# Kernel optimization log

Hardware: AMD Instinct MI355X
Metric: run time of the kernel (lower is better)

## Reference

```python
import jax, jax.numpy as jnp
import numpy as np

B, L_DEC, L_ENC = 4, 1024, 1024
D_MODEL, D_INNER, N_HEAD, D_K, D_V = 512, 256, 8, 64, 64
TEMP = D_K ** 0.5
EPS = 1e-6


def _layernorm(x, g, b):
    mu = jnp.mean(x, axis=-1, keepdims=True)
    var = jnp.mean(jnp.square(x - mu), axis=-1, keepdims=True)
    return (x - mu) * jax.lax.rsqrt(var + EPS) * g + b


def _mha(x_q, x_kv, Wq, Wk, Wv, Wfc, ln_g, ln_b, mask):
    # Faithful to source: only the query input is layer-normed; k/v use raw x_kv.
    resid = x_q
    qn = _layernorm(x_q, ln_g, ln_b)
    # Stacked per-head projections: Wq/Wk/Wv are [H, d_k, d_model]
    q = jnp.einsum('bld,hkd->bhlk', qn, Wq) / TEMP   # [B,H,Lq,dk]
    k = jnp.einsum('bld,hkd->bhlk', x_kv, Wk)        # [B,H,Lk,dk]
    v = jnp.einsum('bld,hkd->bhlk', x_kv, Wv)        # [B,H,Lk,dv]
    scores = jnp.einsum('bhqd,bhkd->bhqk', q, k)     # [B,H,Lq,Lk]
    if mask is not None:
        scores = jnp.where(mask[:, None, :, :] == 0, -jnp.inf, scores)
    attn = jax.nn.softmax(scores, axis=-1)
    out = jnp.einsum('bhqk,bhkd->bhqd', attn, v)     # [B,H,Lq,dv]
    Bq, H, Lq, dv = out.shape
    out = out.transpose(0, 2, 1, 3).reshape(Bq, Lq, H * dv)
    return out @ Wfc.T + resid


def _ffn(x, W1, b1, W2, b2, ln_g, ln_b):
    resid = x
    h = _layernorm(x, ln_g, ln_b)
    h = jax.nn.relu(h @ W1.T + b1) @ W2.T + b2
    return h + resid


def setup_inputs() -> dict:
    key = jax.random.key(0)
    ks = jax.random.split(key, 20)
    s = 0.02
    dec_input = jax.random.normal(ks[0], (B, L_DEC, D_MODEL), jnp.float32)
    enc_output = jax.random.normal(ks[1], (B, L_ENC, D_MODEL), jnp.float32)
    slf_attn_mask = jnp.tril(jnp.ones((1, L_DEC, L_DEC), jnp.int32))  # causal
    p = {}
    for i, pre in enumerate(['slf', 'enc']):
        base = 2 + i * 4
        p[f'{pre}_Wq'] = jax.random.normal(ks[base], (N_HEAD, D_K, D_MODEL), jnp.float32) * s
        p[f'{pre}_Wk'] = jax.random.normal(ks[base + 1], (N_HEAD, D_K, D_MODEL), jnp.float32) * s
        p[f'{pre}_Wv'] = jax.random.normal(ks[base + 2], (N_HEAD, D_V, D_MODEL), jnp.float32) * s
        p[f'{pre}_Wfc'] = jax.random.normal(ks[base + 3], (D_MODEL, N_HEAD * D_V), jnp.float32) * s
        p[f'{pre}_ln_g'] = jnp.ones((D_MODEL,), jnp.float32)
        p[f'{pre}_ln_b'] = jnp.zeros((D_MODEL,), jnp.float32)
    p['ffn_W1'] = jax.random.normal(ks[10], (D_INNER, D_MODEL), jnp.float32) * s
    p['ffn_b1'] = jnp.zeros((D_INNER,), jnp.float32)
    p['ffn_W2'] = jax.random.normal(ks[11], (D_MODEL, D_INNER), jnp.float32) * s
    p['ffn_b2'] = jnp.zeros((D_MODEL,), jnp.float32)
    p['ffn_ln_g'] = jnp.ones((D_MODEL,), jnp.float32)
    p['ffn_ln_b'] = jnp.zeros((D_MODEL,), jnp.float32)
    return {'dec_input': dec_input, 'enc_output': enc_output,
            'slf_attn_mask': slf_attn_mask, **p}


def reference(dec_input, enc_output,
              slf_Wq, slf_Wk, slf_Wv, slf_Wfc, slf_ln_g, slf_ln_b,
              enc_Wq, enc_Wk, enc_Wv, enc_Wfc, enc_ln_g, enc_ln_b,
              ffn_W1, ffn_b1, ffn_W2, ffn_b2, ffn_ln_g, ffn_ln_b,
              slf_attn_mask):
    x = _mha(dec_input, dec_input, slf_Wq, slf_Wk, slf_Wv, slf_Wfc,
             slf_ln_g, slf_ln_b, slf_attn_mask)
    x = _mha(x, enc_output, enc_Wq, enc_Wk, enc_Wv, enc_Wfc,
             enc_ln_g, enc_ln_b, None)
    x = _ffn(x, ffn_W1, ffn_b1, ffn_W2, ffn_b2, ffn_ln_g, ffn_ln_b)
    return x
```

## Files before the change

kernel.cpp:

```cpp
#include <hip/hip_runtime.h>
#include <hip/hip_bf16.h>
#include <math.h>

#define DMODEL 512
#define NHEAD  8
#define DHEAD  64

typedef __attribute__((ext_vector_type(8))) short bf16x8;
typedef __attribute__((ext_vector_type(4))) float f32x4;
typedef __attribute__((ext_vector_type(4))) short short4v;

static __device__ inline short f2bf(float f) {
    __hip_bfloat16 h = __float2bfloat16(f);
    return *reinterpret_cast<short*>(&h);
}

#define GLOAD_LDS16(gp, lp)                                                      \
    __builtin_amdgcn_global_load_lds(                                            \
        (const __attribute__((address_space(1))) unsigned int*)(gp),             \
        (__attribute__((address_space(3))) unsigned int*)(lp), 16, 0, 0)

struct CvtArgs {
    const float* src[10];
    short*       dst[10];
    int          n[10];
};

__global__ __launch_bounds__(256) void cvt_kernel(CvtArgs args) {
    int t = blockIdx.y;
    int idx = (blockIdx.x * 256 + threadIdx.x) * 8;
    if (idx >= args.n[t]) return;
    const float* s = args.src[t] + idx;
    float4 a = *(const float4*)s;
    float4 b = *(const float4*)(s + 4);
    bf16x8 o;
    o[0] = f2bf(a.x); o[1] = f2bf(a.y); o[2] = f2bf(a.z); o[3] = f2bf(a.w);
    o[4] = f2bf(b.x); o[5] = f2bf(b.y); o[6] = f2bf(b.z); o[7] = f2bf(b.w);
    *(bf16x8*)(args.dst[t] + idx) = o;
}

__global__ __launch_bounds__(256) void ln_kernel(const float* __restrict__ X,
                                                 const float* __restrict__ gam,
                                                 const float* __restrict__ bet,
                                                 short* __restrict__ Y,
                                                 const float* __restrict__ C1s,
                                                 short* __restrict__ C1d,
                                                 const float* __restrict__ C2s,
                                                 short* __restrict__ C2d) {
    int row = blockIdx.x * 4 + (threadIdx.x >> 6);
    int tid = threadIdx.x & 63;
    const float* x = X + (size_t)row * DMODEL;
    float4 a = *(const float4*)(x + tid * 4);
    float4 b = *(const float4*)(x + 256 + tid * 4);
    float sum = a.x + a.y + a.z + a.w + b.x + b.y + b.z + b.w;
    float sq  = a.x*a.x + a.y*a.y + a.z*a.z + a.w*a.w
              + b.x*b.x + b.y*b.y + b.z*b.z + b.w*b.w;
#pragma unroll
    for (int off = 1; off < 64; off <<= 1) {
        sum += __shfl_xor(sum, off);
        sq  += __shfl_xor(sq, off);
    }
    float mu  = sum * (1.0f / DMODEL);
    float var = sq * (1.0f / DMODEL) - mu * mu;
    float r   = rsqrtf(var + 1e-6f);

    float4 g1 = *(const float4*)(gam + tid * 4);
    float4 c1 = *(const float4*)(bet + tid * 4);
    float4 g2 = *(const float4*)(gam + 256 + tid * 4);
    float4 c2 = *(const float4*)(bet + 256 + tid * 4);
    short4v y1, y2;
    y1.x = f2bf((a.x - mu) * r * g1.x + c1.x);
    y1.y = f2bf((a.y - mu) * r * g1.y + c1.y);
    y1.z = f2bf((a.z - mu) * r * g1.z + c1.z);
    y1.w = f2bf((a.w - mu) * r * g1.w + c1.w);
    y2.x = f2bf((b.x - mu) * r * g2.x + c2.x);
    y2.y = f2bf((b.y - mu) * r * g2.y + c2.y);
    y2.z = f2bf((b.z - mu) * r * g2.z + c2.z);
    y2.w = f2bf((b.w - mu) * r * g2.w + c2.w);
    short* y = Y + (size_t)row * DMODEL;
    *(short4v*)(y + tid * 4)       = y1;
    *(short4v*)(y + 256 + tid * 4) = y2;

    if (C1s) {
        short4v d1, d2;
        d1.x = f2bf(a.x); d1.y = f2bf(a.y); d1.z = f2bf(a.z); d1.w = f2bf(a.w);
        d2.x = f2bf(b.x); d2.y = f2bf(b.y); d2.z = f2bf(b.z); d2.w = f2bf(b.w);
        short* d = C1d + (size_t)row * DMODEL;
        *(short4v*)(d + tid * 4)       = d1;
        *(short4v*)(d + 256 + tid * 4) = d2;
    }
    if (C2s) {
        const float* e = C2s + (size_t)row * DMODEL;
        float4 ea = *(const float4*)(e + tid * 4);
        float4 eb = *(const float4*)(e + 256 + tid * 4);
        short4v d1, d2;
        d1.x = f2bf(ea.x); d1.y = f2bf(ea.y); d1.z = f2bf(ea.z); d1.w = f2bf(ea.w);
        d2.x = f2bf(eb.x); d2.y = f2bf(eb.y); d2.z = f2bf(eb.z); d2.w = f2bf(eb.w);
        short* d = C2d + (size_t)row * DMODEL;
        *(short4v*)(d + tid * 4)       = d1;
        *(short4v*)(d + 256 + tid * 4) = d2;
    }
}

struct GJobs {
    const short* A[3];
    const short* W[3];
    const float* bias[3];
    const float* resid[3];
    void*        C[3];
    int M[3], N[3], K[3];
    float scale[3];
    int relu[3], obf[3], nblk[3];
};

__global__ __launch_bounds__(256) void gemm_bf16(GJobs jb) {
    __shared__ short As[2][64 * 64];
    __shared__ short Bs[2][64 * 64];

    int bid = blockIdx.x, j = 0;
    while (j < 2 && bid >= jb.nblk[j]) { bid -= jb.nblk[j]; ++j; }
    const short* __restrict__ A = jb.A[j];
    const short* __restrict__ W = jb.W[j];
    const int N = jb.N[j], K = jb.K[j];
    const int nbx = N >> 6;
    const int tn = (bid % nbx) * 64;
    const int tm = (bid / nbx) * 64;

    const int tid  = threadIdx.x;
    const int w    = tid >> 6;
    const int l    = tid & 63;
    const int lq   = l & 15;
    const int g    = l >> 4;
    const int wm   = (w >> 1) * 32;
    const int wn   = (w & 1) * 32;
    const int lrow = l >> 3;
    const int lsl  = l & 7;

    f32x4 acc[2][2];
#pragma unroll
    for (int i = 0; i < 2; ++i)
#pragma unroll
        for (int jj = 0; jj < 2; ++jj)
            acc[i][jj] = (f32x4){0.f, 0.f, 0.f, 0.f};

#define GSTAGE(buf, koff)                                                        \
    do {                                                                         \
        _Pragma("unroll")                                                        \
        for (int i_ = 0; i_ < 2; ++i_) {                                         \
            int row_ = i_ * 32 + w * 8 + lrow;                                   \
            int slot_ = lsl ^ (row_ & 7);                                        \
            GLOAD_LDS16(A + (size_t)(tm + row_) * K + (koff) + slot_ * 8,        \
                        As[buf] + i_ * 2048 + w * 512);                          \
            GLOAD_LDS16(W + (size_t)(tn + row_) * K + (koff) + slot_ * 8,        \
                        Bs[buf] + i_ * 2048 + w * 512);                          \
        }                                                                        \
    } while (0)

    GSTAGE(0, 0);
    int buf = 0;
#pragma unroll 1
    for (int k0 = 0; k0 < K; k0 += 64, buf ^= 1) {
        __syncthreads();
        if (k0 + 64 < K) GSTAGE(buf ^ 1, k0 + 64);
#pragma unroll
        for (int ks = 0; ks < 2; ++ks) {
            const int sl = ((ks * 4 + g) ^ (lq & 7)) * 8;
            bf16x8 af[2], bfv[2];
#pragma unroll
            for (int i = 0; i < 2; ++i) {
                af[i]  = *(const bf16x8*)&As[buf][(wm + i * 16 + lq) * 64 + sl];
                bfv[i] = *(const bf16x8*)&Bs[buf][(wn + i * 16 + lq) * 64 + sl];
            }
#pragma unroll
            for (int i = 0; i < 2; ++i)
#pragma unroll
                for (int jj = 0; jj < 2; ++jj)
                    acc[i][jj] = __builtin_amdgcn_mfma_f32_16x16x32_bf16(
                        af[i], bfv[jj], acc[i][jj], 0, 0, 0);
        }
    }
#undef GSTAGE

    const float* bias  = jb.bias[j];
    const float* resid = jb.resid[j];
    const float scale  = jb.scale[j];
    const int relu = jb.relu[j], obf = jb.obf[j];
#pragma unroll
    for (int i = 0; i < 2; ++i) {
#pragma unroll
        for (int r = 0; r < 4; ++r) {
            int row = tm + wm + i * 16 + g * 4 + r;
#pragma unroll
            for (int jj = 0; jj < 2; ++jj) {
                int col = tn + wn + jj * 16 + lq;
                float v = acc[i][jj][r] * scale;
                if (bias)  v += bias[col];
                if (resid) v += resid[(size_t)row * N + col];
                if (relu)  v = fmaxf(v, 0.f);
                if (obf) ((short*)jb.C[j])[(size_t)row * N + col] = f2bf(v);
                else     ((float*)jb.C[j])[(size_t)row * N + col] = v;
            }
        }
    }
}

__global__ __launch_bounds__(256) void attn_mfma_kernel(
        const short* __restrict__ Q, const short* __restrict__ K,
        const short* __restrict__ V, short* __restrict__ O,
        int Lq, int Lk, int causal, int qs, int kvs) {
    __shared__ short Kt[64 * 64];
    __shared__ short Vt[64][72];
    __shared__ short Pb[4][16][72];

    const int tid  = threadIdx.x;
    const int wave = tid >> 6;
    const int lane = tid & 63;
    const int lq   = lane & 15;
    const int g    = lane >> 4;
    const int bh   = blockIdx.y;
    const int b = bh >> 3, h = bh & 7;
    const int band = causal ? ((bh < 16) ? (int)blockIdx.x : (15 - (int)blockIdx.x))
                            : (int)blockIdx.x;
    const int qt = band * 4 + wave;
    const int q0 = qt * 16;
    const float NEG = -__builtin_inff();

    size_t qoff = (size_t)(b * Lq + q0 + lq) * qs + h * DHEAD;
    bf16x8 qf0 = *(const bf16x8*)(Q + qoff + g * 8);
    bf16x8 qf1 = *(const bf16x8*)(Q + qoff + 32 + g * 8);

    f32x4 o[4] = {{0,0,0,0},{0,0,0,0},{0,0,0,0},{0,0,0,0}};
    f32x4 lacc = {0.f, 0.f, 0.f, 0.f};

    bf16x8 ones;
    {
        short ov = (lq == 0) ? (short)0x3F80 : (short)0;
#pragma unroll
        for (int i = 0; i < 8; ++i) ones[i] = ov;
    }

    const int nkt = causal ? (band + 1) : (Lk >> 6);
    const int lrow = lane >> 3;
    const int lsl  = lane & 7;
    const int va = tid & 31;
    const int vd = (tid >> 5) * 8;

#pragma unroll 1
    for (int kt = 0; kt < nkt; ++kt) {
        __syncthreads();
#pragma unroll
        for (int i = 0; i < 2; ++i) {
            int row = i * 32 + wave * 8 + lrow;
            int slot = lsl ^ (row & 7);
            GLOAD_LDS16(K + (size_t)(b * Lk + kt * 64 + row) * kvs + h * DHEAD + slot * 8,
                        Kt + i * 2048 + wave * 512);
        }
        {
            size_t gb = (size_t)(b * Lk + kt * 64 + 2 * va) * kvs + h * DHEAD + vd;
            bf16x8 v0 = *(const bf16x8*)(V + gb);
            bf16x8 v1 = *(const bf16x8*)(V + gb + kvs);
#pragma unroll
            for (int i = 0; i < 8; ++i) {
                unsigned p = (unsigned short)v0[i] | ((unsigned)(unsigned short)v1[i] << 16);
                *(unsigned*)&Vt[vd + i][2 * va] = p;
            }
        }
        __syncthreads();

        f32x4 s[4];
#pragma unroll
        for (int sub = 0; sub < 4; ++sub) {
            int rr = sub * 16 + lq;
            const int sl0 = ((0 + g) ^ (lq & 7)) * 8;
            const int sl1 = ((4 + g) ^ (lq & 7)) * 8;
            bf16x8 kf0 = *(const bf16x8*)&Kt[rr * 64 + sl0];
            bf16x8 kf1 = *(const bf16x8*)&Kt[rr * 64 + sl1];
            f32x4 a = {0.f, 0.f, 0.f, 0.f};
            a = __builtin_amdgcn_mfma_f32_16x16x32_bf16(kf0, qf0, a, 0, 0, 0);
            a = __builtin_amdgcn_mfma_f32_16x16x32_bf16(kf1, qf1, a, 0, 0, 0);
            s[sub] = a;
        }
        if (causal && kt == nkt - 1) {
            int qg = q0 + lq;
#pragma unroll
            for (int sub = 0; sub < 4; ++sub) {
#pragma unroll
                for (int r = 0; r < 4; ++r) {
                    int kg = kt * 64 + sub * 16 + g * 4 + r;
                    if (kg > qg) s[sub][r] = NEG;
                }
            }
        }

#pragma unroll
        for (int sub = 0; sub < 4; ++sub) {
            short4v p4;
            p4.x = f2bf(__expf(fminf(s[sub][0], 60.f)));
            p4.y = f2bf(__expf(fminf(s[sub][1], 60.f)));
            p4.z = f2bf(__expf(fminf(s[sub][2], 60.f)));
            p4.w = f2bf(__expf(fminf(s[sub][3], 60.f)));
            *(short4v*)&Pb[wave][lq][sub * 16 + g * 4] = p4;
        }
        bf16x8 pf0 = *(const bf16x8*)&Pb[wave][lq][g * 8];
        bf16x8 pf1 = *(const bf16x8*)&Pb[wave][lq][32 + g * 8];

#pragma unroll
        for (int dc = 0; dc < 4; ++dc) {
            bf16x8 vf0 = *(const bf16x8*)&Vt[dc * 16 + lq][g * 8];
            bf16x8 vf1 = *(const bf16x8*)&Vt[dc * 16 + lq][32 + g * 8];
            o[dc] = __builtin_amdgcn_mfma_f32_16x16x32_bf16(pf0, vf0, o[dc], 0, 0, 0);
            o[dc] = __builtin_amdgcn_mfma_f32_16x16x32_bf16(pf1, vf1, o[dc], 0, 0, 0);
        }
        lacc = __builtin_amdgcn_mfma_f32_16x16x32_bf16(pf0, ones, lacc, 0, 0, 0);
        lacc = __builtin_amdgcn_mfma_f32_16x16x32_bf16(pf1, ones, lacc, 0, 0, 0);
    }

#pragma unroll
    for (int r = 0; r < 4; ++r) {
        float lr = __shfl(lacc[r], g << 4);
        float inv = 1.f / lr;
        size_t ob = (size_t)(b * Lq + q0 + g * 4 + r) * qs + h * DHEAD + lq;
        O[ob + 0]  = f2bf(o[0][r] * inv);
        O[ob + 16] = f2bf(o[1][r] * inv);
        O[ob + 32] = f2bf(o[2][r] * inv);
        O[ob + 48] = f2bf(o[3][r] * inv);
    }
}

static void launch_gemm(GJobs& jb, int njobs, hipStream_t stream) {
    int total = 0;
    for (int i = 0; i < 3; ++i) { if (i >= njobs) jb.nblk[i] = 0; total += jb.nblk[i]; }
    gemm_bf16<<<total, 256, 0, stream>>>(jb);
}

extern "C" void kernel_launch(void* const* d_in, const int* in_sizes, int n_in,
                              void* d_out, int out_size, void* d_ws, size_t ws_size,
                              hipStream_t stream) {
    const float* dec       = (const float*)d_in[0];
    const float* enc       = (const float*)d_in[1];
    const float* slf_Wq    = (const float*)d_in[3];
    const float* slf_Wk    = (const float*)d_in[4];
    const float* slf_Wv    = (const float*)d_in[5];
    const float* slf_Wfc   = (const float*)d_in[6];
    const float* slf_ln_g  = (const float*)d_in[7];
    const float* slf_ln_b  = (const float*)d_in[8];
    const float* enc_Wq    = (const float*)d_in[9];
    const float* enc_Wk    = (const float*)d_in[10];
    const float* enc_Wv    = (const float*)d_in[11];
    const float* enc_Wfc   = (const float*)d_in[12];
    const float* enc_ln_g  = (const float*)d_in[13];
    const float* enc_ln_b  = (const float*)d_in[14];
    const float* ffn_W1    = (const float*)d_in[15];
    const float* ffn_b1    = (const float*)d_in[16];
    const float* ffn_W2    = (const float*)d_in[17];
    const float* ffn_b2    = (const float*)d_in[18];
    const float* ffn_ln_g  = (const float*)d_in[19];
    const float* ffn_ln_b  = (const float*)d_in[20];
    float* out = (float*)d_out;

    const int Bb = 4, L = 1024, M = Bb * L;
    const size_t NE = (size_t)M * DMODEL;
    const int WQN = NHEAD * DHEAD * DMODEL;
    float* ws = (float*)d_ws;
    float* x1 = ws;
    float* x2 = ws + NE;
    short* kv16e = (short*)x2;
    short* sb = (short*)(ws + 2 * NE);
    short* dec16 = sb;               sb += NE;
    short* enc16 = sb;               sb += NE;
    short* qn16  = sb;               sb += NE;
    short* q16   = sb;               sb += NE;
    short* ao16  = sb;               sb += NE;
    short* kv16  = sb;               sb += 2 * NE;
    short* h16   = sb;               sb += NE / 2;
    short* wq_s  = sb;               sb += WQN;
    short* wkv_s = sb;               sb += 2 * WQN;
    short* wfc_s = sb;               sb += WQN;
    short* wq_e  = sb;               sb += WQN;
    short* wkv_e = sb;               sb += 2 * WQN;
    short* wfc_e = sb;               sb += WQN;
    short* w1_16 = sb;               sb += 256 * DMODEL;
    short* w2_16 = sb;               sb += DMODEL * 256;

    CvtArgs ca;
    ca.src[0] = slf_Wq;  ca.dst[0] = wq_s;          ca.n[0] = WQN;
    ca.src[1] = slf_Wk;  ca.dst[1] = wkv_s;         ca.n[1] = WQN;
    ca.src[2] = slf_Wv;  ca.dst[2] = wkv_s + WQN;   ca.n[2] = WQN;
    ca.src[3] = slf_Wfc; ca.dst[3] = wfc_s;         ca.n[3] = WQN;
    ca.src[4] = enc_Wq;  ca.dst[4] = wq_e;          ca.n[4] = WQN;
    ca.src[5] = enc_Wk;  ca.dst[5] = wkv_e;         ca.n[5] = WQN;
    ca.src[6] = enc_Wv;  ca.dst[6] = wkv_e + WQN;   ca.n[6] = WQN;
    ca.src[7] = enc_Wfc; ca.dst[7] = wfc_e;         ca.n[7] = WQN;
    ca.src[8] = ffn_W1;  ca.dst[8] = w1_16;         ca.n[8] = 256 * DMODEL;
    ca.src[9] = ffn_W2;  ca.dst[9] = w2_16;         ca.n[9] = DMODEL * 256;
    cvt_kernel<<<dim3(128, 10), 256, 0, stream>>>(ca);

    dim3 attn_grid(L / 64, Bb * NHEAD);
    const int NB512  = (M / 64) * (512 / 64);
    const int NB1024 = (M / 64) * (1024 / 64);
    const int NB256  = (M / 64) * (256 / 64);

    ln_kernel<<<M / 4, 256, 0, stream>>>(dec, slf_ln_g, slf_ln_b, qn16,
                                         dec, dec16, enc, enc16);
    {
        GJobs jb = {};
        jb.A[0] = qn16;  jb.W[0] = wq_s;  jb.C[0] = q16;
        jb.M[0] = M; jb.N[0] = 512;  jb.K[0] = 512; jb.scale[0] = 0.125f;
        jb.obf[0] = 1; jb.nblk[0] = NB512;
        jb.A[1] = dec16; jb.W[1] = wkv_s; jb.C[1] = kv16;
        jb.M[1] = M; jb.N[1] = 1024; jb.K[1] = 512; jb.scale[1] = 1.f;
        jb.obf[1] = 1; jb.nblk[1] = NB1024;
        jb.A[2] = enc16; jb.W[2] = wkv_e; jb.C[2] = kv16e;
        jb.M[2] = M; jb.N[2] = 1024; jb.K[2] = 512; jb.scale[2] = 1.f;
        jb.obf[2] = 1; jb.nblk[2] = NB1024;
        launch_gemm(jb, 3, stream);
    }
    attn_mfma_kernel<<<attn_grid, 256, 0, stream>>>(q16, kv16, kv16 + 512, ao16,
                                                    L, L, 1, DMODEL, 1024);
    {
        GJobs jb = {};
        jb.A[0] = ao16; jb.W[0] = wfc_s; jb.resid[0] = dec; jb.C[0] = x1;
        jb.M[0] = M; jb.N[0] = 512; jb.K[0] = 512; jb.scale[0] = 1.f;
        jb.obf[0] = 0; jb.nblk[0] = NB512;
        launch_gemm(jb, 1, stream);
    }

    ln_kernel<<<M / 4, 256, 0, stream>>>(x1, enc_ln_g, enc_ln_b, qn16,
                                         nullptr, nullptr, nullptr, nullptr);
    {
        GJobs jb = {};
        jb.A[0] = qn16; jb.W[0] = wq_e; jb.C[0] = q16;
        jb.M[0] = M; jb.N[0] = 512; jb.K[0] = 512; jb.scale[0] = 0.125f;
        jb.obf[0] = 1; jb.nblk[0] = NB512;
        launch_gemm(jb, 1, stream);
    }
    attn_mfma_kernel<<<attn_grid, 256, 0, stream>>>(q16, kv16e, kv16e + 512, ao16,
                                                    L, L, 0, DMODEL, 1024);
    {
        GJobs jb = {};
        jb.A[0] = ao16; jb.W[0] = wfc_e; jb.resid[0] = x1; jb.C[0] = x2;
        jb.M[0] = M; jb.N[0] = 512; jb.K[0] = 512; jb.scale[0] = 1.f;
        jb.obf[0] = 0; jb.nblk[0] = NB512;
        launch_gemm(jb, 1, stream);
    }

    ln_kernel<<<M / 4, 256, 0, stream>>>(x2, ffn_ln_g, ffn_ln_b, qn16,
                                         nullptr, nullptr, nullptr, nullptr);
    {
        GJobs jb = {};
        jb.A[0] = qn16; jb.W[0] = w1_16; jb.bias[0] = ffn_b1; jb.C[0] = h16;
        jb.M[0] = M; jb.N[0] = 256; jb.K[0] = 512; jb.scale[0] = 1.f;
        jb.relu[0] = 1; jb.obf[0] = 1; jb.nblk[0] = NB256;
        launch_gemm(jb, 1, stream);
    }
    {
        GJobs jb = {};
        jb.A[0] = h16; jb.W[0] = w2_16; jb.bias[0] = ffn_b2; jb.resid[0] = x2;
        jb.C[0] = out;
        jb.M[0] = M; jb.N[0] = 512; jb.K[0] = 256; jb.scale[0] = 1.f;
        jb.obf[0] = 0; jb.nblk[0] = NB512;
        launch_gemm(jb, 1, stream);
    }
}
```

Measured before the change: 255.6 us.

## Enlarge GEMM tiles, double-buffer attention K/V, use exp2 with folded log2e

GEMM tiles grow from 64x64 to 128x128, with each wave now computing a 64x64 sub-tile of 4x4 MFMAs. The aim is more operand reuse per LDS load, at the cost of more registers and many fewer blocks (e.g. 128 for N=512 with M=4096), which may underfill the device. The attention kernel double-buffers K and V in shared memory, prefetching the next tile while computing the current one, which drops one barrier per iteration. The softmax uses exp2 with log2(e) folded into the Q projection scale.

```diff
diff --git a/kernel.cpp b/kernel.cpp
--- a/kernel.cpp
+++ b/kernel.cpp
@@ -114,39 +114,39 @@
 };
 
 __global__ __launch_bounds__(256) void gemm_bf16(GJobs jb) {
-    __shared__ short As[2][64 * 64];
-    __shared__ short Bs[2][64 * 64];
+    __shared__ short As[2][128 * 64];
+    __shared__ short Bs[2][128 * 64];
 
     int bid = blockIdx.x, j = 0;
     while (j < 2 && bid >= jb.nblk[j]) { bid -= jb.nblk[j]; ++j; }
     const short* __restrict__ A = jb.A[j];
     const short* __restrict__ W = jb.W[j];
     const int N = jb.N[j], K = jb.K[j];
-    const int nbx = N >> 6;
-    const int tn = (bid % nbx) * 64;
-    const int tm = (bid / nbx) * 64;
+    const int nbx = N >> 7;
+    const int tn = (bid % nbx) * 128;
+    const int tm = (bid / nbx) * 128;
 
     const int tid  = threadIdx.x;
     const int w    = tid >> 6;
     const int l    = tid & 63;
     const int lq   = l & 15;
     const int g    = l >> 4;
-    const int wm   = (w >> 1) * 32;
-    const int wn   = (w & 1) * 32;
+    const int w0   = (w >> 1) * 64;
+    const int w1   = (w & 1) * 64;
     const int lrow = l >> 3;
     const int lsl  = l & 7;
 
-    f32x4 acc[2][2];
-#pragma unroll
-    for (int i = 0; i < 2; ++i)
-#pragma unroll
-        for (int jj = 0; jj < 2; ++jj)
+    f32x4 acc[4][4];
+#pragma unroll
+    for (int i = 0; i < 4; ++i)
+#pragma unroll
+        for (int jj = 0; jj < 4; ++jj)
             acc[i][jj] = (f32x4){0.f, 0.f, 0.f, 0.f};
 
 #define GSTAGE(buf, koff)                                                        \
     do {                                                                         \
         _Pragma("unroll")                                                        \
-        for (int i_ = 0; i_ < 2; ++i_) {                                         \
+        for (int i_ = 0; i_ < 4; ++i_) {                                         \
             int row_ = i_ * 32 + w * 8 + lrow;                                   \
             int slot_ = lsl ^ (row_ & 7);                                        \
             GLOAD_LDS16(A + (size_t)(tm + row_) * K + (koff) + slot_ * 8,        \
@@ -165,16 +165,16 @@
 #pragma unroll
         for (int ks = 0; ks < 2; ++ks) {
             const int sl = ((ks * 4 + g) ^ (lq & 7)) * 8;
-            bf16x8 af[2], bfv[2];
-#pragma unroll
-            for (int i = 0; i < 2; ++i) {
-                af[i]  = *(const bf16x8*)&As[buf][(wm + i * 16 + lq) * 64 + sl];
-                bfv[i] = *(const bf16x8*)&Bs[buf][(wn + i * 16 + lq) * 64 + sl];
+            bf16x8 af[4], bfv[4];
+#pragma unroll
+            for (int i = 0; i < 4; ++i) {
+                af[i]  = *(const bf16x8*)&As[buf][(w0 + i * 16 + lq) * 64 + sl];
+                bfv[i] = *(const bf16x8*)&Bs[buf][(w1 + i * 16 + lq) * 64 + sl];
             }
 #pragma unroll
-            for (int i = 0; i < 2; ++i)
-#pragma unroll
-                for (int jj = 0; jj < 2; ++jj)
+            for (int i = 0; i < 4; ++i)
+#pragma unroll
+                for (int jj = 0; jj < 4; ++jj)
                     acc[i][jj] = __builtin_amdgcn_mfma_f32_16x16x32_bf16(
                         af[i], bfv[jj], acc[i][jj], 0, 0, 0);
         }
@@ -186,13 +186,13 @@
     const float scale  = jb.scale[j];
     const int relu = jb.relu[j], obf = jb.obf[j];
 #pragma unroll
-    for (int i = 0; i < 2; ++i) {
+    for (int i = 0; i < 4; ++i) {
 #pragma unroll
         for (int r = 0; r < 4; ++r) {
-            int row = tm + wm + i * 16 + g * 4 + r;
-#pragma unroll
-            for (int jj = 0; jj < 2; ++jj) {
-                int col = tn + wn + jj * 16 + lq;
+            int row = tm + w0 + i * 16 + g * 4 + r;
+#pragma unroll
+            for (int jj = 0; jj < 4; ++jj) {
+                int col = tn + w1 + jj * 16 + lq;
                 float v = acc[i][jj][r] * scale;
                 if (bias)  v += bias[col];
                 if (resid) v += resid[(size_t)row * N + col];
@@ -208,8 +208,8 @@
         const short* __restrict__ Q, const short* __restrict__ K,
         const short* __restrict__ V, short* __restrict__ O,
         int Lq, int Lk, int causal, int qs, int kvs) {
-    __shared__ short Kt[64 * 64];
-    __shared__ short Vt[64][72];
+    __shared__ short Kt[2][64 * 64];
+    __shared__ short Vt[2][64][72];
     __shared__ short Pb[4][16][72];
 
     const int tid  = threadIdx.x;
@@ -245,27 +245,38 @@
     const int va = tid & 31;
     const int vd = (tid >> 5) * 8;
 
-#pragma unroll 1
-    for (int kt = 0; kt < nkt; ++kt) {
-        __syncthreads();
+    bf16x8 vr0, vr1;
+    auto stageK = [&](int kt, int bf) {
 #pragma unroll
         for (int i = 0; i < 2; ++i) {
             int row = i * 32 + wave * 8 + lrow;
             int slot = lsl ^ (row & 7);
             GLOAD_LDS16(K + (size_t)(b * Lk + kt * 64 + row) * kvs + h * DHEAD + slot * 8,
-                        Kt + i * 2048 + wave * 512);
-        }
-        {
-            size_t gb = (size_t)(b * Lk + kt * 64 + 2 * va) * kvs + h * DHEAD + vd;
-            bf16x8 v0 = *(const bf16x8*)(V + gb);
-            bf16x8 v1 = *(const bf16x8*)(V + gb + kvs);
-#pragma unroll
-            for (int i = 0; i < 8; ++i) {
-                unsigned p = (unsigned short)v0[i] | ((unsigned)(unsigned short)v1[i] << 16);
-                *(unsigned*)&Vt[vd + i][2 * va] = p;
-            }
-        }
-        __syncthreads();
+                        Kt[bf] + i * 2048 + wave * 512);
+        }
+    };
+    auto loadV = [&](int kt) {
+        size_t gb = (size_t)(b * Lk + kt * 64 + 2 * va) * kvs + h * DHEAD + vd;
+        vr0 = *(const bf16x8*)(V + gb);
+        vr1 = *(const bf16x8*)(V + gb + kvs);
+    };
+    auto writeV = [&](int bf) {
+#pragma unroll
+        for (int i = 0; i < 8; ++i) {
+            unsigned p = (unsigned short)vr0[i] | ((unsigned)(unsigned short)vr1[i] << 16);
+            *(unsigned*)&Vt[bf][vd + i][2 * va] = p;
+        }
+    };
+
+    stageK(0, 0);
+    loadV(0);
+    writeV(0);
+    __syncthreads();
+
+#pragma unroll 1
+    for (int kt = 0; kt < nkt; ++kt) {
+        const int cur = kt & 1;
+        if (kt + 1 < nkt) { stageK(kt + 1, cur ^ 1); loadV(kt + 1); }
 
         f32x4 s[4];
 #pragma unroll
@@ -273,8 +284,8 @@
             int rr = sub * 16 + lq;
             const int sl0 = ((0 + g) ^ (lq & 7)) * 8;
             const int sl1 = ((4 + g) ^ (lq & 7)) * 8;
-            bf16x8 kf0 = *(const bf16x8*)&Kt[rr * 64 + sl0];
-            bf16x8 kf1 = *(const bf16x8*)&Kt[rr * 64 + sl1];
+            bf16x8 kf0 = *(const bf16x8*)&Kt[cur][rr * 64 + sl0];
+            bf16x8 kf1 = *(const bf16x8*)&Kt[cur][rr * 64 + sl1];
             f32x4 a = {0.f, 0.f, 0.f, 0.f};
             a = __builtin_amdgcn_mfma_f32_16x16x32_bf16(kf0, qf0, a, 0, 0, 0);
             a = __builtin_amdgcn_mfma_f32_16x16x32_bf16(kf1, qf1, a, 0, 0, 0);
@@ -295,10 +306,10 @@
 #pragma unroll
         for (int sub = 0; sub < 4; ++sub) {
             short4v p4;
-            p4.x = f2bf(__expf(fminf(s[sub][0], 60.f)));
-            p4.y = f2bf(__expf(fminf(s[sub][1], 60.f)));
-            p4.z = f2bf(__expf(fminf(s[sub][2], 60.f)));
-            p4.w = f2bf(__expf(fminf(s[sub][3], 60.f)));
+            p4.x = f2bf(exp2f(fminf(s[sub][0], 85.f)));
+            p4.y = f2bf(exp2f(fminf(s[sub][1], 85.f)));
+            p4.z = f2bf(exp2f(fminf(s[sub][2], 85.f)));
+            p4.w = f2bf(exp2f(fminf(s[sub][3], 85.f)));
             *(short4v*)&Pb[wave][lq][sub * 16 + g * 4] = p4;
         }
         bf16x8 pf0 = *(const bf16x8*)&Pb[wave][lq][g * 8];
@@ -306,13 +317,16 @@
 
 #pragma unroll
         for (int dc = 0; dc < 4; ++dc) {
-            bf16x8 vf0 = *(const bf16x8*)&Vt[dc * 16 + lq][g * 8];
-            bf16x8 vf1 = *(const bf16x8*)&Vt[dc * 16 + lq][32 + g * 8];
+            bf16x8 vf0 = *(const bf16x8*)&Vt[cur][dc * 16 + lq][g * 8];
+            bf16x8 vf1 = *(const bf16x8*)&Vt[cur][dc * 16 + lq][32 + g * 8];
             o[dc] = __builtin_amdgcn_mfma_f32_16x16x32_bf16(pf0, vf0, o[dc], 0, 0, 0);
             o[dc] = __builtin_amdgcn_mfma_f32_16x16x32_bf16(pf1, vf1, o[dc], 0, 0, 0);
         }
         lacc = __builtin_amdgcn_mfma_f32_16x16x32_bf16(pf0, ones, lacc, 0, 0, 0);
         lacc = __builtin_amdgcn_mfma_f32_16x16x32_bf16(pf1, ones, lacc, 0, 0, 0);
+
+        if (kt + 1 < nkt) writeV(cur ^ 1);
+        __syncthreads();
     }
 
 #pragma unroll
@@ -361,6 +375,7 @@
     const int Bb = 4, L = 1024, M = Bb * L;
     const size_t NE = (size_t)M * DMODEL;
     const int WQN = NHEAD * DHEAD * DMODEL;
+    const float QSCALE = 0.125f * 1.44269504f;
     float* ws = (float*)d_ws;
     float* x1 = ws;
     float* x2 = ws + NE;
@@ -396,16 +411,16 @@
     cvt_kernel<<<dim3(128, 10), 256, 0, stream>>>(ca);
 
     dim3 attn_grid(L / 64, Bb * NHEAD);
-    const int NB512  = (M / 64) * (512 / 64);
-    const int NB1024 = (M / 64) * (1024 / 64);
-    const int NB256  = (M / 64) * (256 / 64);
+    const int NB512  = (M / 128) * (512 / 128);
+    const int NB1024 = (M / 128) * (1024 / 128);
+    const int NB256  = (M / 128) * (256 / 128);
 
     ln_kernel<<<M / 4, 256, 0, stream>>>(dec, slf_ln_g, slf_ln_b, qn16,
                                          dec, dec16, enc, enc16);
     {
         GJobs jb = {};
         jb.A[0] = qn16;  jb.W[0] = wq_s;  jb.C[0] = q16;
-        jb.M[0] = M; jb.N[0] = 512;  jb.K[0] = 512; jb.scale[0] = 0.125f;
+        jb.M[0] = M; jb.N[0] = 512;  jb.K[0] = 512; jb.scale[0] = QSCALE;
         jb.obf[0] = 1; jb.nblk[0] = NB512;
         jb.A[1] = dec16; jb.W[1] = wkv_s; jb.C[1] = kv16;
         jb.M[1] = M; jb.N[1] = 1024; jb.K[1] = 512; jb.scale[1] = 1.f;
@@ -430,7 +445,7 @@
     {
         GJobs jb = {};
         jb.A[0] = qn16; jb.W[0] = wq_e; jb.C[0] = q16;
-        jb.M[0] = M; jb.N[0] = 512; jb.K[0] = 512; jb.scale[0] = 0.125f;
+        jb.M[0] = M; jb.N[0] = 512; jb.K[0] = 512; jb.scale[0] = QSCALE;
         jb.obf[0] = 1; jb.nblk[0] = NB512;
         launch_gemm(jb, 1, stream);
     }
```

Result: slower. 322.2 us (+26.1%).
